# Performance work log

Hardware: AMD Instinct MI355X
Metric: run time of the kernel (lower is better)

The kernel has to match this reference:

```python
import jax, jax.numpy as jnp
import numpy as np

N_USERS, N_ITEMS, N_CATS, DIM, N_LAYERS = 100000, 50000, 1000, 64, 3
NE_UI, NE_UU, NE_IC = 2000000, 1000000, 150000


def _spmm(rows, cols, vals, H, n_out):
    # sparse [n_out, n_in] @ dense [n_in, D] via gather + segment-sum
    return jax.ops.segment_sum(vals[:, None] * H[cols], rows, num_segments=n_out)


def setup_inputs() -> dict:
    key = jax.random.key(0)
    ks = jax.random.split(key, 16)
    inp = {
        'user_emb': 0.01 * jax.random.normal(ks[0], (N_USERS, DIM), jnp.float32),
        'item_emb': 0.01 * jax.random.normal(ks[1], (N_ITEMS, DIM), jnp.float32),
        'cat_emb': 0.01 * jax.random.normal(ks[2], (N_CATS, DIM), jnp.float32),
        'ui_vals': jax.random.uniform(ks[3], (NE_UI,), jnp.float32),
        'iu_vals': jax.random.uniform(ks[4], (NE_UI,), jnp.float32),
        'uu_vals': jax.random.uniform(ks[5], (NE_UU,), jnp.float32),
        'ic_vals': jax.random.uniform(ks[6], (NE_IC,), jnp.float32),
        'ci_vals': jax.random.uniform(ks[7], (NE_IC,), jnp.float32),
        'ui_rows': jax.random.randint(ks[8], (NE_UI,), 0, N_USERS, jnp.int32),
        'ui_cols': jax.random.randint(ks[9], (NE_UI,), 0, N_ITEMS, jnp.int32),
        'iu_rows': jax.random.randint(ks[10], (NE_UI,), 0, N_ITEMS, jnp.int32),
        'iu_cols': jax.random.randint(ks[11], (NE_UI,), 0, N_USERS, jnp.int32),
        'uu_rows': jax.random.randint(ks[12], (NE_UU,), 0, N_USERS, jnp.int32),
        'uu_cols': jax.random.randint(ks[13], (NE_UU,), 0, N_USERS, jnp.int32),
        'ic_rows': jax.random.randint(ks[14], (NE_IC,), 0, N_ITEMS, jnp.int32),
        'ic_cols': jax.random.randint(ks[15], (NE_IC,), 0, N_CATS, jnp.int32),
        'ci_rows': jax.random.randint(jax.random.fold_in(key, 100), (NE_IC,), 0, N_CATS, jnp.int32),
        'ci_cols': jax.random.randint(jax.random.fold_in(key, 101), (NE_IC,), 0, N_ITEMS, jnp.int32),
    }
    return inp


def reference(user_emb, item_emb, cat_emb, ui_vals, iu_vals, uu_vals, ic_vals, ci_vals,
              ui_rows, ui_cols, iu_rows, iu_cols, uu_rows, uu_cols,
              ic_rows, ic_cols, ci_rows, ci_cols):
    h_u, h_i, h_c = user_emb, item_emb, cat_emb
    sum_u, sum_i = h_u, h_i  # layer-0 contributions
    for _ in range(N_LAYERS):
        new_h_u = (_spmm(ui_rows, ui_cols, ui_vals, h_i, N_USERS)
                   + _spmm(uu_rows, uu_cols, uu_vals, h_u, N_USERS))
        new_h_i = (_spmm(iu_rows, iu_cols, iu_vals, h_u, N_ITEMS)
                   + _spmm(ic_rows, ic_cols, ic_vals, h_c, N_ITEMS))
        new_h_c = _spmm(ci_rows, ci_cols, ci_vals, h_i, N_CATS)
        h_u, h_i, h_c = new_h_u, new_h_i, new_h_c
        sum_u = sum_u + h_u
        sum_i = sum_i + h_i
    inv = 1.0 / (N_LAYERS + 1)
    return sum_u * inv, sum_i * inv, h_c
```

## Files before the change

### kernel.cpp

```cpp
#include <hip/hip_runtime.h>

typedef unsigned int uint;
typedef unsigned short ushort;

constexpr int DIM      = 64;
constexpr int N_USERS  = 100000;
constexpr int N_ITEMS  = 50000;
constexpr int N_CATS   = 1000;
constexpr int NE_UI    = 2000000;
constexpr int NE_UU    = 1000000;
constexpr int NE_IC    = 150000;
constexpr int N_LAYERS = 3;

constexpr int ROW_U0    = N_ITEMS;
constexpr int ROW_C0    = N_ITEMS + N_USERS;
constexpr int TOT_ROWS  = ROW_C0 + N_CATS;
constexpr size_t TOT_EL = (size_t)TOT_ROWS * DIM;

constexpr int NE_USERS = NE_UI + NE_UU;
constexpr int NE_ITEMS = NE_UI + NE_IC;
constexpr int NE_CATS  = NE_IC;

constexpr int SH_U = 9, SH_I = 8, SH_C = 2;
constexpr int NB_U = (N_USERS + 511) / 512;
constexpr int NB_I = (N_ITEMS + 255) / 256;
constexpr int NB_C = (N_CATS + 3) / 4;
constexpr int CHUNK = 8192;
constexpr int CH_U = (NE_USERS + CHUNK - 1) / CHUNK;
constexpr int CH_I = (NE_ITEMS + CHUNK - 1) / CHUNK;
constexpr int CH_C = (NE_CATS  + CHUNK - 1) / CHUNK;

constexpr int COLSHIFT = 18;
constexpr int COLMASK  = 0x3FFFF;

constexpr int CAST_BLKS = 1024;


__device__ __forceinline__ ushort f2bf(float f) {
    uint u = __float_as_uint(f);
    u += 0x7FFFu + ((u >> 16) & 1u);
    return (ushort)(u >> 16);
}
__device__ __forceinline__ float bfl(uint u) { return __uint_as_float(u << 16); }
__device__ __forceinline__ float bfh(uint u) { return __uint_as_float(u & 0xFFFF0000u); }


struct RelSrc {
    const int* rowsA; const int* colsA; const float* valsA; int neA; int offA;
    const int* rowsB; const int* colsB; const float* valsB; int neB; int offB;
    int shift; int n_out;
};

struct BuildParams {
    RelSrc rel[3];
    int* bcnt;
    int* boffs;
    int* cursor;
    int2* bucketed[3];
    int* ptr[3];
    int2* edges[3];
};

__global__ __launch_bounds__(256) void fused_cast_hist(BuildParams P,
                                                       const float* __restrict__ ue,
                                                       const float* __restrict__ ie,
                                                       const float* __restrict__ ce,
                                                       ushort* __restrict__ H) {
    int bid = blockIdx.x;
    if (bid < CAST_BLKS) {
        constexpr int NI8 = (N_ITEMS * DIM) / 8;
        constexpr int NU8 = (N_USERS * DIM) / 8;
        constexpr int NC8 = (N_CATS  * DIM) / 8;
        constexpr int TOT8 = NI8 + NU8 + NC8;
        int st = CAST_BLKS * 256;
        for (int i = bid * 256 + threadIdx.x; i < TOT8; i += st) {
            const float* src; int s8;
            if (i < NI8)            { src = ie; s8 = i; }
            else if (i < NI8 + NU8) { src = ue; s8 = i - NI8; }
            else                    { src = ce; s8 = i - NI8 - NU8; }
            float4 a = reinterpret_cast<const float4*>(src)[2 * s8];
            float4 b = reinterpret_cast<const float4*>(src)[2 * s8 + 1];
            uint4 v;
            v.x = (uint)f2bf(a.x) | ((uint)f2bf(a.y) << 16);
            v.y = (uint)f2bf(a.z) | ((uint)f2bf(a.w) << 16);
            v.z = (uint)f2bf(b.x) | ((uint)f2bf(b.y) << 16);
            v.w = (uint)f2bf(b.z) | ((uint)f2bf(b.w) << 16);
            reinterpret_cast<uint4*>(H)[i] = v;
        }
    } else {
        int b2 = bid - CAST_BLKS;
        int rel = b2 >> 8;
        int lbk = b2 & 255;
        RelSrc R = P.rel[rel];
        __shared__ int lb[256];
        lb[threadIdx.x] = 0;
        __syncthreads();
        int ne = R.neA + R.neB;
        for (int i = lbk * 256 + threadIdx.x; i < ne; i += 256 * 256) {
            int r = (i < R.neA) ? R.rowsA[i] : R.rowsB[i - R.neA];
            atomicAdd(&lb[r >> R.shift], 1);
        }
        __syncthreads();
        if (lb[threadIdx.x]) atomicAdd(&P.bcnt[rel * 256 + threadIdx.x], lb[threadIdx.x]);
    }
}

__global__ void fused_scan(const int* __restrict__ bcnt, int* __restrict__ boffs,
                           int* __restrict__ cursor) {
    __shared__ int lds[256];
    int rel = blockIdx.x, tid = threadIdx.x;
    int v = bcnt[rel * 256 + tid];
    lds[tid] = v;
    __syncthreads();
    for (int off = 1; off < 256; off <<= 1) {
        int t = (tid >= off) ? lds[tid - off] : 0;
        __syncthreads();
        lds[tid] += t;
        __syncthreads();
    }
    int excl = lds[tid] - v;
    boffs[rel * 257 + tid] = excl;
    cursor[rel * 256 + tid] = excl;
    if (tid == 255) boffs[rel * 257 + 256] = lds[255];
}

__global__ __launch_bounds__(1024) void fused_scatter(BuildParams P, int c0, int c01) {
    __shared__ int2 stage[CHUNK];
    __shared__ unsigned char sb[CHUNK];
    __shared__ int hist[256], lbase[256], gbase[256], cnt[256];
    int bid = blockIdx.x, tid = threadIdx.x;
    int rel = (bid < c0) ? 0 : ((bid < c01) ? 1 : 2);
    int ch  = bid - ((rel == 0) ? 0 : ((rel == 1) ? c0 : c01));
    RelSrc R = P.rel[rel];
    int ne = R.neA + R.neB;
    int base = ch * CHUNK;
    int nedge = min(CHUNK, ne - base);
    int* cursor = P.cursor + rel * 256;
    int2* out = P.bucketed[rel];

    if (tid < 256) hist[tid] = 0;
    __syncthreads();
    for (int k = tid; k < nedge; k += 1024) {
        int gi = base + k;
        int r = (gi < R.neA) ? R.rowsA[gi] : R.rowsB[gi - R.neA];
        atomicAdd(&hist[r >> R.shift], 1);
    }
    __syncthreads();
    if (tid < 256) lbase[tid] = hist[tid];
    __syncthreads();
    for (int off = 1; off < 256; off <<= 1) {
        int t = (tid < 256 && tid >= off) ? lbase[tid - off] : 0;
        __syncthreads();
        if (tid < 256) lbase[tid] += t;
        __syncthreads();
    }
    if (tid < 256) {
        int excl = lbase[tid] - hist[tid];
        cnt[tid] = excl;
        gbase[tid] = hist[tid] ? atomicAdd(&cursor[tid], hist[tid]) : 0;
        lbase[tid] = excl;
    }
    __syncthreads();
    for (int k = tid; k < nedge; k += 1024) {
        int gi = base + k;
        int r, c; float v;
        if (gi < R.neA) { r = R.rowsA[gi]; c = R.colsA[gi] + R.offA; v = R.valsA[gi]; }
        else { int q = gi - R.neA; r = R.rowsB[q]; c = R.colsB[q] + R.offB; v = R.valsB[q]; }
        int b = r >> R.shift;
        int slot = atomicAdd(&cnt[b], 1);
        int lr = r - (b << R.shift);
        stage[slot] = make_int2((lr << COLSHIFT) | c, __float_as_int(v));
        sb[slot] = (unsigned char)b;
    }
    __syncthreads();
    for (int j = tid; j < nedge; j += 1024) {
        int b = sb[j];
        out[gbase[b] + (j - lbase[b])] = stage[j];
    }
}

__global__ __launch_bounds__(256) void fused_finalize(BuildParams P, int nb0, int nb01,
                                                      int nbu, int nbi, int nbc) {
    __shared__ int h[512], psum[256], cur[512];
    int bg = blockIdx.x, tid = threadIdx.x;
    int rel = (bg < nb0) ? 0 : ((bg < nb01) ? 1 : 2);
    int lb  = bg - ((rel == 0) ? 0 : ((rel == 1) ? nb0 : nb01));
    int nb  = (rel == 0) ? nbu : ((rel == 1) ? nbi : nbc);
    RelSrc R = P.rel[rel];
    const int* boffs = P.boffs + rel * 257;
    const int2* bucketed = P.bucketed[rel];
    int* ptr = P.ptr[rel];
    int2* edges = P.edges[rel];

    int s = boffs[lb], e = boffs[lb + 1];
    int base_row = lb << R.shift;
    int nrows_b = min(1 << R.shift, R.n_out - base_row);
    h[tid] = 0; h[tid + 256] = 0;
    __syncthreads();
    for (int j = s + tid; j < e; j += 256)
        atomicAdd(&h[(unsigned)bucketed[j].x >> COLSHIFT], 1);
    __syncthreads();
    int a0 = h[2 * tid], a1 = h[2 * tid + 1];
    psum[tid] = a0 + a1;
    __syncthreads();
    for (int off = 1; off < 256; off <<= 1) {
        int t = (tid >= off) ? psum[tid - off] : 0;
        __syncthreads();
        psum[tid] += t;
        __syncthreads();
    }
    int pex = (tid == 0) ? 0 : psum[tid - 1];
    cur[2 * tid] = pex;
    cur[2 * tid + 1] = pex + a0;
    if (2 * tid < nrows_b)     ptr[base_row + 2 * tid]     = s + pex;
    if (2 * tid + 1 < nrows_b) ptr[base_row + 2 * tid + 1] = s + pex + a0;
    if (lb == nb - 1 && tid == 0) ptr[R.n_out] = boffs[nb];
    __syncthreads();
    for (int j = s + tid; j < e; j += 256) {
        int2 w = bucketed[j];
        int lr = (unsigned)w.x >> COLSHIFT;
        int slot = atomicAdd(&cur[lr], 1);
        edges[s + slot] = make_int2((w.x & COLMASK) << 7, w.y);
    }
}


__device__ __forceinline__ void fma8(uint4 hv, float w, float* acc) {
    acc[0] = fmaf(w, bfl(hv.x), acc[0]);
    acc[1] = fmaf(w, bfh(hv.x), acc[1]);
    acc[2] = fmaf(w, bfl(hv.y), acc[2]);
    acc[3] = fmaf(w, bfh(hv.y), acc[3]);
    acc[4] = fmaf(w, bfl(hv.z), acc[4]);
    acc[5] = fmaf(w, bfh(hv.z), acc[5]);
    acc[6] = fmaf(w, bfl(hv.w), acc[6]);
    acc[7] = fmaf(w, bfh(hv.w), acc[7]);
}

__device__ __forceinline__ void gather8(const int* __restrict__ ptr,
                                        const int2* __restrict__ edges,
                                        const ushort* __restrict__ H,
                                        int r, int grp, int sub, float* acc) {
    int s = ptr[r], e = ptr[r + 1];
    const char* Hb = (const char*)H + sub * 16;
    for (int j0 = s + grp; j0 < e; j0 += 32) {
        int j1 = j0 + 8, j2 = j0 + 16, j3 = j0 + 24;
        int2 e0 = edges[j0];
        int2 e1 = edges[j1 < e ? j1 : j0];
        int2 e2 = edges[j2 < e ? j2 : j0];
        int2 e3 = edges[j3 < e ? j3 : j0];
        uint4 h0 = *reinterpret_cast<const uint4*>(Hb + e0.x);
        uint4 h1 = *reinterpret_cast<const uint4*>(Hb + e1.x);
        uint4 h2 = *reinterpret_cast<const uint4*>(Hb + e2.x);
        uint4 h3 = *reinterpret_cast<const uint4*>(Hb + e3.x);
        float w1 = (j1 < e) ? __int_as_float(e1.y) : 0.f;
        float w2 = (j2 < e) ? __int_as_float(e2.y) : 0.f;
        float w3 = (j3 < e) ? __int_as_float(e3.y) : 0.f;
        fma8(h0, __int_as_float(e0.y), acc);
        fma8(h1, w1, acc);
        fma8(h2, w2, acc);
        fma8(h3, w3, acc);
    }
}

__device__ __forceinline__ void xreduce8(float* a) {
#pragma unroll
    for (int m = 8; m <= 32; m <<= 1)
#pragma unroll
        for (int k = 0; k < 8; ++k)
            a[k] += __shfl_xor(a[k], m);
}

__device__ __forceinline__ uint4 pack_bf8(const float* a) {
    uint4 v;
    v.x = (uint)f2bf(a[0]) | ((uint)f2bf(a[1]) << 16);
    v.y = (uint)f2bf(a[2]) | ((uint)f2bf(a[3]) << 16);
    v.z = (uint)f2bf(a[4]) | ((uint)f2bf(a[5]) << 16);
    v.w = (uint)f2bf(a[6]) | ((uint)f2bf(a[7]) << 16);
    return v;
}

__global__ void fused_layer(const int* __restrict__ u_ptr, const int2* __restrict__ u_e,
                            const int* __restrict__ i_ptr, const int2* __restrict__ i_e,
                            const int* __restrict__ c_ptr, const int2* __restrict__ c_e,
                            const ushort* __restrict__ Hcur, ushort* __restrict__ Hnxt,
                            float* __restrict__ sum_u, float* __restrict__ sum_i,
                            float* __restrict__ out_c,
                            const float* __restrict__ user_emb, const float* __restrict__ item_emb,
                            float scale, int first, int last) {
    int wid  = (blockIdx.x * blockDim.x + threadIdx.x) >> 6;
    int lane = threadIdx.x & 63;
    if (wid >= TOT_ROWS) return;
    int grp = lane >> 3, sub = lane & 7;
    float acc[8] = {0.f, 0.f, 0.f, 0.f, 0.f, 0.f, 0.f, 0.f};
    const int* ptr; const int2* eg; int lr;
    if (wid < ROW_U0)      { ptr = i_ptr; eg = i_e; lr = wid; }
    else if (wid < ROW_C0) { ptr = u_ptr; eg = u_e; lr = wid - ROW_U0; }
    else                   { ptr = c_ptr; eg = c_e; lr = wid - ROW_C0; }
    gather8(ptr, eg, Hcur, lr, grp, sub, acc);
    xreduce8(acc);
    size_t o = (size_t)wid * DIM + sub * 8;
    if (wid < ROW_C0) {
        float* sum; const float* emb; size_t so;
        if (wid < ROW_U0) { sum = sum_i; emb = item_emb; so = o; }
        else { sum = sum_u; emb = user_emb; so = (size_t)lr * DIM + sub * 8; }
        const float4* bp = reinterpret_cast<const float4*>((first ? emb : (const float*)sum) + so);
        if (last) {
            if (grp == 0) {
                float4 s0 = bp[0], s1 = bp[1];
                s0.x = (s0.x + acc[0]) * scale; s0.y = (s0.y + acc[1]) * scale;
                s0.z = (s0.z + acc[2]) * scale; s0.w = (s0.w + acc[3]) * scale;
                s1.x = (s1.x + acc[4]) * scale; s1.y = (s1.y + acc[5]) * scale;
                s1.z = (s1.z + acc[6]) * scale; s1.w = (s1.w + acc[7]) * scale;
                float4* sp = reinterpret_cast<float4*>(sum + so);
                sp[0] = s0; sp[1] = s1;
            }
        } else {
            if (grp == 0) {
                *reinterpret_cast<uint4*>(Hnxt + o) = pack_bf8(acc);
            } else if (grp == 1) {
                float4 s0 = bp[0], s1 = bp[1];
                s0.x += acc[0]; s0.y += acc[1]; s0.z += acc[2]; s0.w += acc[3];
                s1.x += acc[4]; s1.y += acc[5]; s1.z += acc[6]; s1.w += acc[7];
                float4* sp = reinterpret_cast<float4*>(sum + so);
                sp[0] = s0; sp[1] = s1;
            }
        }
    } else {
        if (grp != 0) return;
        if (last) {
            float4* op = reinterpret_cast<float4*>(out_c + (size_t)lr * DIM + sub * 8);
            op[0] = make_float4(acc[0], acc[1], acc[2], acc[3]);
            op[1] = make_float4(acc[4], acc[5], acc[6], acc[7]);
        } else {
            *reinterpret_cast<uint4*>(Hnxt + o) = pack_bf8(acc);
        }
    }
}


__global__ void spmm_edges(const int* __restrict__ rows, const int* __restrict__ cols,
                           const float* __restrict__ vals, const float* __restrict__ H,
                           float* __restrict__ out, int ne) {
    int tid  = blockIdx.x * blockDim.x + threadIdx.x;
    int e    = tid >> 6;
    int lane = threadIdx.x & 63;
    if (e >= ne) return;
    float x = vals[e] * H[(size_t)cols[e] * DIM + lane];
    unsafeAtomicAdd(&out[(size_t)rows[e] * DIM + lane], x);
}

__global__ void accum_kernel(float* __restrict__ sum, const float* __restrict__ h, int n) {
    int i = blockIdx.x * blockDim.x + threadIdx.x;
    int st = gridDim.x * blockDim.x;
    for (; i < n; i += st) sum[i] += h[i];
}

__global__ void scale_kernel(float* __restrict__ p, int n, float s) {
    int i = blockIdx.x * blockDim.x + threadIdx.x;
    int st = gridDim.x * blockDim.x;
    for (; i < n; i += st) p[i] *= s;
}


extern "C" void kernel_launch(void* const* d_in, const int* in_sizes, int n_in,
                              void* d_out, int out_size, void* d_ws, size_t ws_size,
                              hipStream_t stream) {
    const float* user_emb = (const float*)d_in[0];
    const float* item_emb = (const float*)d_in[1];
    const float* cat_emb  = (const float*)d_in[2];
    const float* ui_vals  = (const float*)d_in[3];
    const float* iu_vals  = (const float*)d_in[4];
    const float* uu_vals  = (const float*)d_in[5];
    const float* ic_vals  = (const float*)d_in[6];
    const float* ci_vals  = (const float*)d_in[7];
    const int*   ui_rows  = (const int*)d_in[8];
    const int*   ui_cols  = (const int*)d_in[9];
    const int*   iu_rows  = (const int*)d_in[10];
    const int*   iu_cols  = (const int*)d_in[11];
    const int*   uu_rows  = (const int*)d_in[12];
    const int*   uu_cols  = (const int*)d_in[13];
    const int*   ic_rows  = (const int*)d_in[14];
    const int*   ic_cols  = (const int*)d_in[15];
    const int*   ci_rows  = (const int*)d_in[16];
    const int*   ci_cols  = (const int*)d_in[17];

    constexpr size_t NU = (size_t)N_USERS * DIM;
    constexpr size_t NI = (size_t)N_ITEMS * DIM;
    constexpr size_t NC = (size_t)N_CATS  * DIM;

    float* sum_u = (float*)d_out;
    float* sum_i = sum_u + NU;
    float* out_c = sum_i + NI;

    const int blk = 256;
    const float inv = 1.0f / (N_LAYERS + 1);

    unsigned char* wb = (unsigned char*)d_ws;
    size_t woff = 0;
    auto take = [&](size_t bytes) -> void* {
        void* p = wb + woff;
        woff = (woff + bytes + 15) & ~(size_t)15;
        return p;
    };
    ushort* Hbuf[2] = { (ushort*)take(TOT_EL * 2), (ushort*)take(TOT_EL * 2) };
    int* u_ptr = (int*)take(((size_t)N_USERS + 1) * 4);
    int* i_ptr = (int*)take(((size_t)N_ITEMS + 1) * 4);
    int* c_ptr = (int*)take(((size_t)N_CATS  + 1) * 4);
    int2* u_e = (int2*)take((size_t)NE_USERS * 8);
    int2* i_e = (int2*)take((size_t)NE_ITEMS * 8);
    int2* c_e = (int2*)take((size_t)NE_CATS  * 8);
    int2* bk_i = (int2*)take((size_t)NE_ITEMS * 8);
    int2* bk_c = (int2*)take((size_t)NE_CATS  * 8);
    int* bcnt   = (int*)take(3 * 256 * 4);
    int* boffs  = (int*)take(3 * 257 * 4);
    int* cursor = (int*)take(3 * 256 * 4);
    size_t needed_bytes = woff;
    int2* bk_u = (int2*)d_out;

    if (ws_size >= needed_bytes) {
        BuildParams P;
        P.rel[0] = { ui_rows, ui_cols, ui_vals, NE_UI, 0,
                     uu_rows, uu_cols, uu_vals, NE_UU, ROW_U0, SH_U, N_USERS };
        P.rel[1] = { iu_rows, iu_cols, iu_vals, NE_UI, ROW_U0,
                     ic_rows, ic_cols, ic_vals, NE_IC, ROW_C0, SH_I, N_ITEMS };
        P.rel[2] = { ci_rows, ci_cols, ci_vals, NE_IC, 0,
                     nullptr, nullptr, nullptr, 0, 0, SH_C, N_CATS };
        P.bcnt = bcnt; P.boffs = boffs; P.cursor = cursor;
        P.bucketed[0] = bk_u; P.bucketed[1] = bk_i; P.bucketed[2] = bk_c;
        P.ptr[0] = u_ptr; P.ptr[1] = i_ptr; P.ptr[2] = c_ptr;
        P.edges[0] = u_e; P.edges[1] = i_e; P.edges[2] = c_e;

        hipMemsetAsync(bcnt, 0, 3 * 256 * sizeof(int), stream);
        fused_cast_hist<<<CAST_BLKS + 3 * 256, blk, 0, stream>>>(P, user_emb, item_emb,
                                                                 cat_emb, Hbuf[0]);
        fused_scan<<<3, blk, 0, stream>>>(bcnt, boffs, cursor);
        fused_scatter<<<CH_U + CH_I + CH_C, 1024, 0, stream>>>(P, CH_U, CH_U + CH_I);
        fused_finalize<<<NB_U + NB_I + NB_C, blk, 0, stream>>>(P, NB_U, NB_U + NB_I,
                                                               NB_U, NB_I, NB_C);

        int grid = (TOT_ROWS * 64 + blk - 1) / blk;
        int cur = 0;
        for (int l = 0; l < N_LAYERS; ++l) {
            int nxt = cur ^ 1;
            fused_layer<<<grid, blk, 0, stream>>>(u_ptr, u_e, i_ptr, i_e, c_ptr, c_e,
                                                  Hbuf[cur], Hbuf[nxt],
                                                  sum_u, sum_i, out_c,
                                                  user_emb, item_emb,
                                                  inv, l == 0, l == N_LAYERS - 1);
            cur = nxt;
        }
    } else {
        float* ws = (float*)d_ws;
        float* f_u[2] = { ws,               ws + NU };
        float* f_i[2] = { ws + 2 * NU,      ws + 2 * NU + NI };
        float* f_c[2] = { ws + 2 * NU + 2 * NI, ws + 2 * NU + 2 * NI + NC };
        hipMemcpyAsync(f_u[0], user_emb, NU * sizeof(float), hipMemcpyDeviceToDevice, stream);
        hipMemcpyAsync(f_i[0], item_emb, NI * sizeof(float), hipMemcpyDeviceToDevice, stream);
        hipMemcpyAsync(f_c[0], cat_emb,  NC * sizeof(float), hipMemcpyDeviceToDevice, stream);
        hipMemcpyAsync(sum_u,  user_emb, NU * sizeof(float), hipMemcpyDeviceToDevice, stream);
        hipMemcpyAsync(sum_i,  item_emb, NI * sizeof(float), hipMemcpyDeviceToDevice, stream);
        const int ew_grid = 2048;
        int cur = 0;
        for (int l = 0; l < N_LAYERS; ++l) {
            int nxt = cur ^ 1;
            hipMemsetAsync(f_u[nxt], 0, NU * sizeof(float), stream);
            hipMemsetAsync(f_i[nxt], 0, NI * sizeof(float), stream);
            hipMemsetAsync(f_c[nxt], 0, NC * sizeof(float), stream);
            spmm_edges<<<(NE_UI + 3) / 4, blk, 0, stream>>>(ui_rows, ui_cols, ui_vals, f_i[cur], f_u[nxt], NE_UI);
            spmm_edges<<<(NE_UU + 3) / 4, blk, 0, stream>>>(uu_rows, uu_cols, uu_vals, f_u[cur], f_u[nxt], NE_UU);
            spmm_edges<<<(NE_UI + 3) / 4, blk, 0, stream>>>(iu_rows, iu_cols, iu_vals, f_u[cur], f_i[nxt], NE_UI);
            spmm_edges<<<(NE_IC + 3) / 4, blk, 0, stream>>>(ic_rows, ic_cols, ic_vals, f_c[cur], f_i[nxt], NE_IC);
            spmm_edges<<<(NE_IC + 3) / 4, blk, 0, stream>>>(ci_rows, ci_cols, ci_vals, f_i[cur], f_c[nxt], NE_IC);
            accum_kernel<<<ew_grid, blk, 0, stream>>>(sum_u, f_u[nxt], (int)NU);
            accum_kernel<<<ew_grid, blk, 0, stream>>>(sum_i, f_i[nxt], (int)NI);
            cur = nxt;
        }
        scale_kernel<<<ew_grid, blk, 0, stream>>>(sum_u, (int)NU, inv);
        scale_kernel<<<ew_grid, blk, 0, stream>>>(sum_i, (int)NI, inv);
        hipMemcpyAsync(out_c, f_c[cur], NC * sizeof(float), hipMemcpyDeviceToDevice, stream);
    }
}
```

Baseline: 412.9 us.

## Defer layer-sum accumulation to last layer and use contiguous per-group edge ranges

Each layer now writes only the bf16 next-hidden buffer, with three rotating buffers kept. The final layer forms the running sum from the fp32 embedding, the two stored bf16 intermediate layers and the current accumulator, which removes the fp32 sum read-modify-write in the earlier layers. The gather also assigns each 8-lane group a contiguous chunk of the row's edges instead of strided interleaving, which can improve edge-array locality but may unbalance short rows. Bucket scratch is aliased onto the extra H buffers, and intermediate sums now come from bf16-rounded values, which lowers precision slightly.

```diff
diff --git a/kernel.cpp b/kernel.cpp
--- a/kernel.cpp
+++ b/kernel.cpp
@@ -241,20 +241,23 @@
                                         const ushort* __restrict__ H,
                                         int r, int grp, int sub, float* acc) {
     int s = ptr[r], e = ptr[r + 1];
+    int L = (e - s + 7) >> 3;
+    int gs = s + grp * L;
+    int ge = min(gs + L, e);
     const char* Hb = (const char*)H + sub * 16;
-    for (int j0 = s + grp; j0 < e; j0 += 32) {
-        int j1 = j0 + 8, j2 = j0 + 16, j3 = j0 + 24;
+    for (int j0 = gs; j0 < ge; j0 += 4) {
+        int j1 = j0 + 1, j2 = j0 + 2, j3 = j0 + 3;
         int2 e0 = edges[j0];
-        int2 e1 = edges[j1 < e ? j1 : j0];
-        int2 e2 = edges[j2 < e ? j2 : j0];
-        int2 e3 = edges[j3 < e ? j3 : j0];
+        int2 e1 = edges[j1 < ge ? j1 : j0];
+        int2 e2 = edges[j2 < ge ? j2 : j0];
+        int2 e3 = edges[j3 < ge ? j3 : j0];
         uint4 h0 = *reinterpret_cast<const uint4*>(Hb + e0.x);
         uint4 h1 = *reinterpret_cast<const uint4*>(Hb + e1.x);
         uint4 h2 = *reinterpret_cast<const uint4*>(Hb + e2.x);
         uint4 h3 = *reinterpret_cast<const uint4*>(Hb + e3.x);
-        float w1 = (j1 < e) ? __int_as_float(e1.y) : 0.f;
-        float w2 = (j2 < e) ? __int_as_float(e2.y) : 0.f;
-        float w3 = (j3 < e) ? __int_as_float(e3.y) : 0.f;
+        float w1 = (j1 < ge) ? __int_as_float(e1.y) : 0.f;
+        float w2 = (j2 < ge) ? __int_as_float(e2.y) : 0.f;
+        float w3 = (j3 < ge) ? __int_as_float(e3.y) : 0.f;
         fma8(h0, __int_as_float(e0.y), acc);
         fma8(h1, w1, acc);
         fma8(h2, w2, acc);
@@ -283,10 +286,11 @@
                             const int* __restrict__ i_ptr, const int2* __restrict__ i_e,
                             const int* __restrict__ c_ptr, const int2* __restrict__ c_e,
                             const ushort* __restrict__ Hcur, ushort* __restrict__ Hnxt,
+                            const ushort* __restrict__ H1, const ushort* __restrict__ H2,
                             float* __restrict__ sum_u, float* __restrict__ sum_i,
                             float* __restrict__ out_c,
                             const float* __restrict__ user_emb, const float* __restrict__ item_emb,
-                            float scale, int first, int last) {
+                            float scale, int last) {
     int wid  = (blockIdx.x * blockDim.x + threadIdx.x) >> 6;
     int lane = threadIdx.x & 63;
     if (wid >= TOT_ROWS) return;
@@ -298,42 +302,33 @@
     else                   { ptr = c_ptr; eg = c_e; lr = wid - ROW_C0; }
     gather8(ptr, eg, Hcur, lr, grp, sub, acc);
     xreduce8(acc);
+    if (grp != 0) return;
     size_t o = (size_t)wid * DIM + sub * 8;
-    if (wid < ROW_C0) {
-        float* sum; const float* emb; size_t so;
-        if (wid < ROW_U0) { sum = sum_i; emb = item_emb; so = o; }
-        else { sum = sum_u; emb = user_emb; so = (size_t)lr * DIM + sub * 8; }
-        const float4* bp = reinterpret_cast<const float4*>((first ? emb : (const float*)sum) + so);
-        if (last) {
-            if (grp == 0) {
-                float4 s0 = bp[0], s1 = bp[1];
-                s0.x = (s0.x + acc[0]) * scale; s0.y = (s0.y + acc[1]) * scale;
-                s0.z = (s0.z + acc[2]) * scale; s0.w = (s0.w + acc[3]) * scale;
-                s1.x = (s1.x + acc[4]) * scale; s1.y = (s1.y + acc[5]) * scale;
-                s1.z = (s1.z + acc[6]) * scale; s1.w = (s1.w + acc[7]) * scale;
-                float4* sp = reinterpret_cast<float4*>(sum + so);
-                sp[0] = s0; sp[1] = s1;
-            }
-        } else {
-            if (grp == 0) {
-                *reinterpret_cast<uint4*>(Hnxt + o) = pack_bf8(acc);
-            } else if (grp == 1) {
-                float4 s0 = bp[0], s1 = bp[1];
-                s0.x += acc[0]; s0.y += acc[1]; s0.z += acc[2]; s0.w += acc[3];
-                s1.x += acc[4]; s1.y += acc[5]; s1.z += acc[6]; s1.w += acc[7];
-                float4* sp = reinterpret_cast<float4*>(sum + so);
-                sp[0] = s0; sp[1] = s1;
-            }
-        }
+    if (!last) {
+        *reinterpret_cast<uint4*>(Hnxt + o) = pack_bf8(acc);
+    } else if (wid < ROW_C0) {
+        const float* emb; float* dst; size_t so;
+        if (wid < ROW_U0) { emb = item_emb; dst = sum_i; so = o; }
+        else { emb = user_emb; dst = sum_u; so = (size_t)lr * DIM + sub * 8; }
+        uint4 a1 = *reinterpret_cast<const uint4*>(H1 + o);
+        uint4 a2 = *reinterpret_cast<const uint4*>(H2 + o);
+        const float4* ep = reinterpret_cast<const float4*>(emb + so);
+        float4 b0 = ep[0], b1 = ep[1];
+        float4 r0, r1;
+        r0.x = (b0.x + bfl(a1.x) + bfl(a2.x) + acc[0]) * scale;
+        r0.y = (b0.y + bfh(a1.x) + bfh(a2.x) + acc[1]) * scale;
+        r0.z = (b0.z + bfl(a1.y) + bfl(a2.y) + acc[2]) * scale;
+        r0.w = (b0.w + bfh(a1.y) + bfh(a2.y) + acc[3]) * scale;
+        r1.x = (b1.x + bfl(a1.z) + bfl(a2.z) + acc[4]) * scale;
+        r1.y = (b1.y + bfh(a1.z) + bfh(a2.z) + acc[5]) * scale;
+        r1.z = (b1.z + bfl(a1.w) + bfl(a2.w) + acc[6]) * scale;
+        r1.w = (b1.w + bfh(a1.w) + bfh(a2.w) + acc[7]) * scale;
+        float4* dp = reinterpret_cast<float4*>(dst + so);
+        dp[0] = r0; dp[1] = r1;
     } else {
-        if (grp != 0) return;
-        if (last) {
-            float4* op = reinterpret_cast<float4*>(out_c + (size_t)lr * DIM + sub * 8);
-            op[0] = make_float4(acc[0], acc[1], acc[2], acc[3]);
-            op[1] = make_float4(acc[4], acc[5], acc[6], acc[7]);
-        } else {
-            *reinterpret_cast<uint4*>(Hnxt + o) = pack_bf8(acc);
-        }
+        float4* op = reinterpret_cast<float4*>(out_c + (size_t)lr * DIM + sub * 8);
+        op[0] = make_float4(acc[0], acc[1], acc[2], acc[3]);
+        op[1] = make_float4(acc[4], acc[5], acc[6], acc[7]);
     }
 }
 
@@ -402,20 +397,21 @@
         woff = (woff + bytes + 15) & ~(size_t)15;
         return p;
     };
-    ushort* Hbuf[2] = { (ushort*)take(TOT_EL * 2), (ushort*)take(TOT_EL * 2) };
+    ushort* Hbuf[3] = { (ushort*)take(TOT_EL * 2), (ushort*)take(TOT_EL * 2),
+                        (ushort*)take(TOT_EL * 2) };
     int* u_ptr = (int*)take(((size_t)N_USERS + 1) * 4);
     int* i_ptr = (int*)take(((size_t)N_ITEMS + 1) * 4);
     int* c_ptr = (int*)take(((size_t)N_CATS  + 1) * 4);
     int2* u_e = (int2*)take((size_t)NE_USERS * 8);
     int2* i_e = (int2*)take((size_t)NE_ITEMS * 8);
     int2* c_e = (int2*)take((size_t)NE_CATS  * 8);
-    int2* bk_i = (int2*)take((size_t)NE_ITEMS * 8);
-    int2* bk_c = (int2*)take((size_t)NE_CATS  * 8);
     int* bcnt   = (int*)take(3 * 256 * 4);
     int* boffs  = (int*)take(3 * 257 * 4);
     int* cursor = (int*)take(3 * 256 * 4);
     size_t needed_bytes = woff;
     int2* bk_u = (int2*)d_out;
+    int2* bk_i = (int2*)Hbuf[1];
+    int2* bk_c = (int2*)Hbuf[2];
 
     if (ws_size >= needed_bytes) {
         BuildParams P;
@@ -439,15 +435,13 @@
                                                                NB_U, NB_I, NB_C);
 
         int grid = (TOT_ROWS * 64 + blk - 1) / blk;
-        int cur = 0;
         for (int l = 0; l < N_LAYERS; ++l) {
-            int nxt = cur ^ 1;
             fused_layer<<<grid, blk, 0, stream>>>(u_ptr, u_e, i_ptr, i_e, c_ptr, c_e,
-                                                  Hbuf[cur], Hbuf[nxt],
+                                                  Hbuf[l], Hbuf[l + 1 < 3 ? l + 1 : 0],
+                                                  Hbuf[1], Hbuf[2],
                                                   sum_u, sum_i, out_c,
                                                   user_emb, item_emb,
-                                                  inv, l == 0, l == N_LAYERS - 1);
-            cur = nxt;
+                                                  inv, l == N_LAYERS - 1);
         }
     } else {
         float* ws = (float*)d_ws;
```

New measurement: 388.1 us (median of 2 runs). 1.06x faster.
